# Kernel optimization log

Measured on AMD Instinct MI355X. Metric: run time of the kernel, lower is better.

## Reference

```python
import jax, jax.numpy as jnp
import numpy as np
import math

B, L, D, H, FF = 4, 1024, 1024, 16, 4096
DH = D // H
EPS = 1e-12


def layer_norm(x, gamma, beta):
    mean = x.mean(-1, keepdims=True)
    var = ((x - mean) ** 2).mean(-1, keepdims=True)  # biased var, matches unbiased=False
    return gamma * (x - mean) / jnp.sqrt(var + EPS) + beta


def setup_inputs() -> dict:
    key = jax.random.key(0)
    ks = jax.random.split(key, 16)
    s = 0.02
    return {
        "x": jax.random.normal(ks[0], (B, L, D), jnp.float32),
        "attn_bias": jax.random.uniform(ks[1], (B, L, L), jnp.float32),
        "src_mask": jax.random.randint(ks[2], (B, L), 0, 2, jnp.int32),
        "wq": jax.random.normal(ks[3], (D, D), jnp.float32) * s,
        "bq": jnp.zeros((D,), jnp.float32),
        "wk": jax.random.normal(ks[4], (D, D), jnp.float32) * s,
        "bk": jnp.zeros((D,), jnp.float32),
        "wv": jax.random.normal(ks[5], (D, D), jnp.float32) * s,
        "bv": jnp.zeros((D,), jnp.float32),
        "wo": jax.random.normal(ks[6], (D, D), jnp.float32) * s,
        "bo": jnp.zeros((D,), jnp.float32),
        "gamma1": jnp.ones((D,), jnp.float32),
        "beta1": jnp.zeros((D,), jnp.float32),
        "w1": jax.random.normal(ks[7], (D, FF), jnp.float32) * s,
        "b1": jnp.zeros((FF,), jnp.float32),
        "w2": jax.random.normal(ks[8], (FF, D), jnp.float32) * s,
        "b2": jnp.zeros((D,), jnp.float32),
        "gamma2": jnp.ones((D,), jnp.float32),
        "beta2": jnp.zeros((D,), jnp.float32),
    }


def reference(x, attn_bias, src_mask, wq, bq, wk, bk, wv, bv, wo, bo,
              gamma1, beta1, w1, b1, w2, b2, gamma2, beta2):
    # ---- multi-head attention with multiplicative bias + additive mask ----
    def split_heads(t):  # [B,L,D] -> [B,H,L,DH]
        return t.reshape(B, L, H, DH).transpose(0, 2, 1, 3)

    q = split_heads(x @ wq + bq)
    k = split_heads(x @ wk + bk)
    v = split_heads(x @ wv + bv)

    score = jnp.einsum('bhqd,bhkd->bhqk', q, k) / math.sqrt(DH)
    score = score * attn_bias[:, None, :, :]               # multiplicative bias
    score = jnp.where(src_mask[:, None, None, :] == 0, -10000.0, score)
    p = jax.nn.softmax(score, axis=-1)
    ctx = jnp.einsum('bhqk,bhkd->bhqd', p, v)
    ctx = ctx.transpose(0, 2, 1, 3).reshape(B, L, D)
    attn_out = ctx @ wo + bo

    h = layer_norm(x + attn_out, gamma1, beta1)

    # ---- position-wise FFN ----
    ffn = jax.nn.relu(h @ w1 + b1) @ w2 + b2
    out = layer_norm(h + ffn, gamma2, beta2)
    return out
```

## Files before the change

kernel.cpp:

```cpp
#include <hip/hip_runtime.h>
#include <hip/hip_bf16.h>
#include <math.h>

#define BB 4
#define LL 1024
#define DD 1024
#define HH 16
#define DHH 64
#define FFF 4096
#define MM (BB*LL)
#define LDQ 3072

typedef __attribute__((ext_vector_type(8))) short short8;
typedef __attribute__((ext_vector_type(4))) float f32x4;

__device__ __forceinline__ ushort f2bf(float f) {
    __hip_bfloat16 h = __float2bfloat16(f);
    return *(ushort*)&h;
}
__device__ __forceinline__ float bf2f(ushort u) {
    __hip_bfloat16 h = *(__hip_bfloat16*)&u;
    return __bfloat162float(h);
}
__device__ __forceinline__ float fexp2(float x) {
#if __has_builtin(__builtin_amdgcn_exp2f)
    return __builtin_amdgcn_exp2f(x);
#else
    return exp2f(x);
#endif
}

__device__ __forceinline__ float block_reduce_sum(float v, float* red, int tid) {
    red[tid] = v;
    __syncthreads();
    for (int off = 128; off > 0; off >>= 1) {
        if (tid < off) red[tid] += red[tid + off];
        __syncthreads();
    }
    float r = red[0];
    __syncthreads();
    return r;
}

__global__ __launch_bounds__(256)
void cast_bf16(const float* __restrict__ in, ushort* __restrict__ out) {
    const int i = blockIdx.x * 256 + threadIdx.x;
    float4 v = ((const float4*)in)[i];
    ushort4 o;
    o.x = f2bf(v.x); o.y = f2bf(v.y); o.z = f2bf(v.z); o.w = f2bf(v.w);
    ((ushort4*)out)[i] = o;
}

__global__ __launch_bounds__(256)
void swizzle_bias(const float* __restrict__ bias, float* __restrict__ B) {
    __shared__ float rowbuf[1024];
    const int row = blockIdx.x;
    const int t = threadIdx.x;
    *(float4*)&rowbuf[t * 4] = *(const float4*)&bias[(size_t)row * 1024 + t * 4];
    __syncthreads();
    const int kt = t >> 4, c = t & 15;
    const float s = 1.4426950408889634f;
    float4 o;
    o.x = rowbuf[kt * 64 + 0 * 16 + c] * s;
    o.y = rowbuf[kt * 64 + 1 * 16 + c] * s;
    o.z = rowbuf[kt * 64 + 2 * 16 + c] * s;
    o.w = rowbuf[kt * 64 + 3 * 16 + c] * s;
    *(float4*)&B[(size_t)row * 1024 + t * 4] = o;
}

__global__ __launch_bounds__(256)
void transpose_cast(const float* __restrict__ W, ushort* __restrict__ WT,
                    int K, int N) {
    __shared__ float tile[32][33];
    const int n0 = blockIdx.x * 32, k0 = blockIdx.y * 32;
    const int t = threadIdx.x;
    const int r = t >> 3, c4 = (t & 7) * 4;
    float4 v = *(const float4*)&W[(size_t)(k0 + r) * N + n0 + c4];
    tile[r][c4 + 0] = v.x; tile[r][c4 + 1] = v.y;
    tile[r][c4 + 2] = v.z; tile[r][c4 + 3] = v.w;
    __syncthreads();
    ushort4 o;
    o.x = f2bf(tile[c4 + 0][r]);
    o.y = f2bf(tile[c4 + 1][r]);
    o.z = f2bf(tile[c4 + 2][r]);
    o.w = f2bf(tile[c4 + 3][r]);
    *(ushort4*)&WT[(size_t)(n0 + r) * K + k0 + c4] = o;
}

__global__ __launch_bounds__(256)
void concat3(const float* __restrict__ a, const float* __restrict__ b,
             const float* __restrict__ c, float* __restrict__ o) {
    const int i = blockIdx.x * 256 + threadIdx.x;
    o[i] = (i < 1024) ? a[i] : ((i < 2048) ? b[i - 1024] : c[i - 2048]);
}

template<int BN>
__global__ __launch_bounds__(256)
void gemm_bf16(const ushort* __restrict__ A, const ushort* __restrict__ Bt,
               const float* __restrict__ bias, void* __restrict__ C,
               ushort* __restrict__ Vt, int vn0,
               int M, int N, int K, int relu, int obf16, int qlim) {
    constexpr int JF = BN / 32;
    __shared__ ushort Als0[128 * 32];
    __shared__ ushort Als1[128 * 32];
    __shared__ ushort Bls0[BN * 32];
    __shared__ ushort Bls1[BN * 32];

    const int L = blockIdx.x + gridDim.x * blockIdx.y;
    const int xcd = L & 7;
    const int idx = L >> 3;
    const int mpx = gridDim.y >> 3;
    const int bm = (xcd * mpx + (idx % mpx)) * 128;
    const int bn = (idx / mpx) * BN;

    const int t = threadIdx.x;
    const int lane = t & 63;
    const int w = t >> 6;
    const int wm = (w >> 1) * 64;
    const int wn = (w & 1) * (BN / 2);
    const int fm = lane & 15;
    const int kg = lane >> 4;

    f32x4 acc[4][JF] = {};

    for (int k0 = 0; k0 < K; k0 += 64) {
        #pragma unroll
        for (int j = 0; j < 2; ++j) {
            const int chunk = j * 256 + t;
            const int row = chunk >> 2, kc = chunk & 3;
            const ushort* ga0 = A + (size_t)(bm + row) * K + k0 + kc * 8;
            __builtin_amdgcn_global_load_lds(
                (const __attribute__((address_space(1))) void*)ga0,
                (__attribute__((address_space(3))) void*)(Als0 + chunk * 8), 16, 0, 0);
            const ushort* ga1 = ga0 + 32;
            __builtin_amdgcn_global_load_lds(
                (const __attribute__((address_space(1))) void*)ga1,
                (__attribute__((address_space(3))) void*)(Als1 + chunk * 8), 16, 0, 0);
        }
        #pragma unroll
        for (int j = 0; j < BN / 64; ++j) {
            const int chunk = j * 256 + t;
            const int row = chunk >> 2, kc = chunk & 3;
            const ushort* gb0 = Bt + (size_t)(bn + row) * K + k0 + kc * 8;
            __builtin_amdgcn_global_load_lds(
                (const __attribute__((address_space(1))) void*)gb0,
                (__attribute__((address_space(3))) void*)(Bls0 + chunk * 8), 16, 0, 0);
            const ushort* gb1 = gb0 + 32;
            __builtin_amdgcn_global_load_lds(
                (const __attribute__((address_space(1))) void*)gb1,
                (__attribute__((address_space(3))) void*)(Bls1 + chunk * 8), 16, 0, 0);
        }
        __syncthreads();

        short8 af[4][2], bfr[JF][2];
        #pragma unroll
        for (int i = 0; i < 4; ++i) {
            af[i][0] = *(const short8*)&Als0[(wm + i * 16 + fm) * 32 + kg * 8];
            af[i][1] = *(const short8*)&Als1[(wm + i * 16 + fm) * 32 + kg * 8];
        }
        #pragma unroll
        for (int j = 0; j < JF; ++j) {
            bfr[j][0] = *(const short8*)&Bls0[(wn + j * 16 + fm) * 32 + kg * 8];
            bfr[j][1] = *(const short8*)&Bls1[(wn + j * 16 + fm) * 32 + kg * 8];
        }
        #pragma unroll
        for (int i = 0; i < 4; ++i)
            #pragma unroll
            for (int j = 0; j < JF; ++j) {
                acc[i][j] = __builtin_amdgcn_mfma_f32_16x16x32_bf16(
                    af[i][0], bfr[j][0], acc[i][j], 0, 0, 0);
                acc[i][j] = __builtin_amdgcn_mfma_f32_16x16x32_bf16(
                    af[i][1], bfr[j][1], acc[i][j], 0, 0, 0);
            }
        __syncthreads();
    }

    const int orow0 = (lane >> 4) * 4;
    const int ocol = lane & 15;
    #pragma unroll
    for (int j = 0; j < JF; ++j) {
        const int n = bn + wn + j * 16 + ocol;
        const float bv = bias[n];
        const bool isV = (bn + wn + j * 16) >= vn0;
        #pragma unroll
        for (int i = 0; i < 4; ++i) {
            const int m0 = bm + wm + i * 16 + orow0;
            if (isV) {
                ushort4 o;
                float v0 = acc[i][j][0] + bv, v1 = acc[i][j][1] + bv;
                float v2 = acc[i][j][2] + bv, v3 = acc[i][j][3] + bv;
                o.x = f2bf(v0); o.y = f2bf(v1); o.z = f2bf(v2); o.w = f2bf(v3);
                *(ushort4*)&Vt[((size_t)((m0 >> 10) << 10) + (n - vn0)) * 1024 + (m0 & 1023)] = o;
            } else {
                #pragma unroll
                for (int r = 0; r < 4; ++r) {
                    const int m = m0 + r;
                    float v = acc[i][j][r] + bv;
                    if (relu) v = fmaxf(v, 0.0f);
                    if (n < qlim) v *= 0.125f;
                    if (obf16)
                        ((ushort*)C)[(size_t)m * N + n] = f2bf(v);
                    else
                        ((float*)C)[(size_t)m * N + n] = v;
                }
            }
        }
    }
}

template<int BN>
__global__ __launch_bounds__(256)
void gemm_bf16_sk(const ushort* __restrict__ A, const ushort* __restrict__ Bt,
                  float* __restrict__ P, int M, int N, int K) {
    constexpr int JF = BN / 32;
    __shared__ ushort Als0[128 * 32];
    __shared__ ushort Als1[128 * 32];
    __shared__ ushort Bls0[BN * 32];
    __shared__ ushort Bls1[BN * 32];

    const int L = blockIdx.x + gridDim.x * blockIdx.y;
    const int xcd = L & 7;
    const int idx = L >> 3;
    const int mpx = gridDim.y >> 3;
    const int bm = (xcd * mpx + (idx % mpx)) * 128;
    const int bn = (idx / mpx) * BN;
    const int kbeg = blockIdx.z * (K >> 1);
    const int kend = kbeg + (K >> 1);

    const int t = threadIdx.x;
    const int lane = t & 63;
    const int w = t >> 6;
    const int wm = (w >> 1) * 64;
    const int wn = (w & 1) * (BN / 2);
    const int fm = lane & 15;
    const int kg = lane >> 4;

    f32x4 acc[4][JF] = {};

    for (int k0 = kbeg; k0 < kend; k0 += 64) {
        #pragma unroll
        for (int j = 0; j < 2; ++j) {
            const int chunk = j * 256 + t;
            const int row = chunk >> 2, kc = chunk & 3;
            const ushort* ga0 = A + (size_t)(bm + row) * K + k0 + kc * 8;
            __builtin_amdgcn_global_load_lds(
                (const __attribute__((address_space(1))) void*)ga0,
                (__attribute__((address_space(3))) void*)(Als0 + chunk * 8), 16, 0, 0);
            const ushort* ga1 = ga0 + 32;
            __builtin_amdgcn_global_load_lds(
                (const __attribute__((address_space(1))) void*)ga1,
                (__attribute__((address_space(3))) void*)(Als1 + chunk * 8), 16, 0, 0);
        }
        #pragma unroll
        for (int j = 0; j < BN / 64; ++j) {
            const int chunk = j * 256 + t;
            const int row = chunk >> 2, kc = chunk & 3;
            const ushort* gb0 = Bt + (size_t)(bn + row) * K + k0 + kc * 8;
            __builtin_amdgcn_global_load_lds(
                (const __attribute__((address_space(1))) void*)gb0,
                (__attribute__((address_space(3))) void*)(Bls0 + chunk * 8), 16, 0, 0);
            const ushort* gb1 = gb0 + 32;
            __builtin_amdgcn_global_load_lds(
                (const __attribute__((address_space(1))) void*)gb1,
                (__attribute__((address_space(3))) void*)(Bls1 + chunk * 8), 16, 0, 0);
        }
        __syncthreads();

        short8 af[4][2], bfr[JF][2];
        #pragma unroll
        for (int i = 0; i < 4; ++i) {
            af[i][0] = *(const short8*)&Als0[(wm + i * 16 + fm) * 32 + kg * 8];
            af[i][1] = *(const short8*)&Als1[(wm + i * 16 + fm) * 32 + kg * 8];
        }
        #pragma unroll
        for (int j = 0; j < JF; ++j) {
            bfr[j][0] = *(const short8*)&Bls0[(wn + j * 16 + fm) * 32 + kg * 8];
            bfr[j][1] = *(const short8*)&Bls1[(wn + j * 16 + fm) * 32 + kg * 8];
        }
        #pragma unroll
        for (int i = 0; i < 4; ++i)
            #pragma unroll
            for (int j = 0; j < JF; ++j) {
                acc[i][j] = __builtin_amdgcn_mfma_f32_16x16x32_bf16(
                    af[i][0], bfr[j][0], acc[i][j], 0, 0, 0);
                acc[i][j] = __builtin_amdgcn_mfma_f32_16x16x32_bf16(
                    af[i][1], bfr[j][1], acc[i][j], 0, 0, 0);
            }
        __syncthreads();
    }

    float* Pz = P + (size_t)blockIdx.z * M * N;
    const int orow0 = (lane >> 4) * 4;
    const int ocol = lane & 15;
    #pragma unroll
    for (int j = 0; j < JF; ++j) {
        const int n = bn + wn + j * 16 + ocol;
        #pragma unroll
        for (int i = 0; i < 4; ++i) {
            const int m0 = bm + wm + i * 16 + orow0;
            #pragma unroll
            for (int r = 0; r < 4; ++r)
                Pz[(size_t)(m0 + r) * N + n] = acc[i][j][r];
        }
    }
}

__global__ __launch_bounds__(256, 4)
void attn_mfma(const ushort* __restrict__ QKVb, const ushort* __restrict__ Vt,
               const float* __restrict__ biasw, const int* __restrict__ mask,
               ushort* __restrict__ ctx) {
    const int q0 = blockIdx.x * 64;
    const int h = blockIdx.y;
    const int b = blockIdx.z;
    const int t = threadIdx.x;
    const int lane = t & 63;
    const int w = t >> 6;
    const int g = lane >> 4;
    const int c = lane & 15;

    __shared__ ushort QP[64 * 72];
    __shared__ ushort Ks[64 * 72];
    __shared__ ushort Vs[64 * 72];
    __shared__ float maskS[LL];

    #pragma unroll
    for (int i = 0; i < 2; ++i) {
        const int chunk = i * 256 + t;
        const int row = chunk >> 3, c8 = (chunk & 7) * 8;
        *(short8*)&QP[row * 72 + c8] =
            *(const short8*)(QKVb + ((size_t)(b * LL + q0 + row)) * LDQ + h * DHH + c8);
    }
    {
        int4 mi = ((const int4*)(mask + b * LL))[t];
        float4 mf;
        mf.x = mi.x ? 0.0f : -49152.0f;
        mf.y = mi.y ? 0.0f : -49152.0f;
        mf.z = mi.z ? 0.0f : -49152.0f;
        mf.w = mi.w ? 0.0f : -49152.0f;
        ((float4*)maskS)[t] = mf;
    }

    short8 pk[2], pv[2];
    #pragma unroll
    for (int i = 0; i < 2; ++i) {
        const int chunk = i * 256 + t;
        const int row = chunk >> 3, c8 = (chunk & 7) * 8;
        pk[i] = *(const short8*)(QKVb + ((size_t)(b * LL + row)) * LDQ + 1024 + h * DHH + c8);
        pv[i] = *(const short8*)(Vt + ((size_t)((b * HH + h) * DHH + row)) * LL + c8);
    }
    __syncthreads();

    short8 aq0 = *(const short8*)&QP[(w * 16 + c) * 72 + g * 8];
    short8 aq1 = *(const short8*)&QP[(w * 16 + c) * 72 + g * 8 + 32];
    ushort* Pw = QP + w * (16 * 72);

    const float* bp = biasw + (size_t)(b * LL + q0 + w * 16 + 4 * g) * 1024 + c * 4;
    float4 pb[4];
    #pragma unroll
    for (int r = 0; r < 4; ++r)
        pb[r] = *(const float4*)(bp + r * 1024);

    float l_run[4] = {0.f, 0.f, 0.f, 0.f};
    f32x4 acc_o[4] = {};

    for (int kt = 0; kt < 16; ++kt) {
        #pragma unroll
        for (int i = 0; i < 2; ++i) {
            const int chunk = i * 256 + t;
            const int row = chunk >> 3, c8 = (chunk & 7) * 8;
            *(short8*)&Ks[row * 72 + c8] = pk[i];
            *(short8*)&Vs[row * 72 + c8] = pv[i];
        }
        __syncthreads();

        if (kt < 15) {
            const int k0n = (kt + 1) * 64;
            #pragma unroll
            for (int i = 0; i < 2; ++i) {
                const int chunk = i * 256 + t;
                const int row = chunk >> 3, c8 = (chunk & 7) * 8;
                pk[i] = *(const short8*)(QKVb + ((size_t)(b * LL + k0n + row)) * LDQ + 1024 + h * DHH + c8);
                pv[i] = *(const short8*)(Vt + ((size_t)((b * HH + h) * DHH + row)) * LL + k0n + c8);
            }
        }

        float4 pbn[4];
        if (kt < 15) {
            #pragma unroll
            for (int r = 0; r < 4; ++r)
                pbn[r] = *(const float4*)(bp + r * 1024 + (kt + 1) * 64);
        }

        float mk[4];
        #pragma unroll
        for (int j = 0; j < 4; ++j) mk[j] = maskS[kt * 64 + j * 16 + c];

        f32x4 accs[4] = {};
        __builtin_amdgcn_s_setprio(1);
        #pragma unroll
        for (int j = 0; j < 4; ++j) {
            short8 bk0 = *(const short8*)&Ks[(j * 16 + c) * 72 + g * 8];
            short8 bk1 = *(const short8*)&Ks[(j * 16 + c) * 72 + g * 8 + 32];
            accs[j] = __builtin_amdgcn_mfma_f32_16x16x32_bf16(aq0, bk0, accs[j], 0, 0, 0);
            accs[j] = __builtin_amdgcn_mfma_f32_16x16x32_bf16(aq1, bk1, accs[j], 0, 0, 0);
        }
        __builtin_amdgcn_s_setprio(0);

        #pragma unroll
        for (int j = 0; j < 4; ++j)
            #pragma unroll
            for (int r = 0; r < 4; ++r) {
                const float pe = fexp2(fmaf(accs[j][r], ((const float*)&pb[r])[j], mk[j]));
                l_run[r] += pe;
                Pw[(4 * g + r) * 72 + j * 16 + c] = f2bf(pe);
            }

        __builtin_amdgcn_s_setprio(1);
        #pragma unroll
        for (int ks = 0; ks < 2; ++ks) {
            short8 ap = *(const short8*)&Pw[c * 72 + ks * 32 + g * 8];
            #pragma unroll
            for (int j = 0; j < 4; ++j) {
                short8 bv8 = *(const short8*)&Vs[(j * 16 + c) * 72 + ks * 32 + g * 8];
                acc_o[j] = __builtin_amdgcn_mfma_f32_16x16x32_bf16(ap, bv8, acc_o[j], 0, 0, 0);
            }
        }
        __builtin_amdgcn_s_setprio(0);

        if (kt < 15) {
            #pragma unroll
            for (int r = 0; r < 4; ++r) pb[r] = pbn[r];
        }
        __syncthreads();
    }

    #pragma unroll
    for (int r = 0; r < 4; ++r) {
        float l = l_run[r];
        #pragma unroll
        for (int d = 1; d < 16; d <<= 1) l += __shfl_xor(l, d);
        const float inv = 1.0f / l;
        #pragma unroll
        for (int j = 0; j < 4; ++j)
            ctx[((size_t)(b * LL + q0 + w * 16 + 4 * g + r)) * DD + h * DHH + j * 16 + c] =
                f2bf(acc_o[j][r] * inv);
    }
}

__global__ __launch_bounds__(256)
void add_ln_kernel(const float* __restrict__ P0, const float* __restrict__ P1,
                   const float* __restrict__ cb, const float* __restrict__ bres,
                   const float* __restrict__ gamma, const float* __restrict__ beta,
                   float* __restrict__ out, ushort* __restrict__ outb) {
    const int row = blockIdx.x;
    const int tid = threadIdx.x;
    __shared__ float red[256];

    const size_t base = (size_t)row * DD;
    float v[4];
    float sum = 0.0f;
    #pragma unroll
    for (int i = 0; i < 4; ++i) {
        const int col = tid + i * 256;
        v[i] = P0[base + col] + P1[base + col] + cb[col] + bres[base + col];
        sum += v[i];
    }
    const float mean = block_reduce_sum(sum, red, tid) * (1.0f / 1024.0f);
    float vs = 0.0f;
    #pragma unroll
    for (int i = 0; i < 4; ++i) {
        const float dlt = v[i] - mean;
        vs += dlt * dlt;
    }
    const float var = block_reduce_sum(vs, red, tid) * (1.0f / 1024.0f);
    const float rstd = rsqrtf(var + 1e-12f);
    #pragma unroll
    for (int i = 0; i < 4; ++i) {
        const int col = tid + i * 256;
        const float o = gamma[col] * (v[i] - mean) * rstd + beta[col];
        out[base + col] = o;
        if (outb) outb[base + col] = f2bf(o);
    }
}

extern "C" void kernel_launch(void* const* d_in, const int* in_sizes, int n_in,
                              void* d_out, int out_size, void* d_ws, size_t ws_size,
                              hipStream_t stream) {
    const float* x         = (const float*)d_in[0];
    const float* attn_bias = (const float*)d_in[1];
    const int*   src_mask  = (const int*)  d_in[2];
    const float* wq = (const float*)d_in[3];
    const float* bq = (const float*)d_in[4];
    const float* wk = (const float*)d_in[5];
    const float* bk = (const float*)d_in[6];
    const float* wv = (const float*)d_in[7];
    const float* bv = (const float*)d_in[8];
    const float* wo = (const float*)d_in[9];
    const float* bo = (const float*)d_in[10];
    const float* gamma1 = (const float*)d_in[11];
    const float* beta1  = (const float*)d_in[12];
    const float* w1 = (const float*)d_in[13];
    const float* b1 = (const float*)d_in[14];
    const float* w2 = (const float*)d_in[15];
    const float* b2 = (const float*)d_in[16];
    const float* gamma2 = (const float*)d_in[17];
    const float* beta2  = (const float*)d_in[18];
    float* out = (float*)d_out;

    const size_t MB = 1024 * 1024;
    char* W = (char*)d_ws;
    ushort* xb    = (ushort*)(W + 0);
    ushort* ctxb  = (ushort*)(W + 0);
    ushort* W1T   = (ushort*)(W + 0);
    ushort* QKVb  = (ushort*)(W + 8 * MB);
    float*  Hb    = (float*) (W + 8 * MB);
    ushort* Hbb   = (ushort*)(W + 24 * MB);
    ushort* W2T   = (ushort*)(W + 24 * MB);
    ushort* F1b   = (ushort*)(W + 32 * MB);
    ushort* Vt    = (ushort*)(W + 40 * MB);
    ushort* WQKVT = (ushort*)(W + 48 * MB);
    ushort* WOT   = (ushort*)(W + 48 * MB);
    float*  bqkv  = (float*) (W + 62 * MB);
    float*  biasw = (float*) (W + 64 * MB);
    float*  P0    = (float*) (W + 64 * MB);

    dim3 blk(256);

    cast_bf16<<<dim3(4096), blk, 0, stream>>>(x, xb);
    swizzle_bias<<<dim3(4096), blk, 0, stream>>>(attn_bias, biasw);
    transpose_cast<<<dim3(32, 32), blk, 0, stream>>>(wq, WQKVT, DD, DD);
    transpose_cast<<<dim3(32, 32), blk, 0, stream>>>(wk, WQKVT + 1024 * 1024, DD, DD);
    transpose_cast<<<dim3(32, 32), blk, 0, stream>>>(wv, WQKVT + 2048 * 1024, DD, DD);
    concat3<<<dim3(12), blk, 0, stream>>>(bq, bk, bv, bqkv);
    gemm_bf16<128><<<dim3(24, 32), blk, 0, stream>>>(xb, WQKVT, bqkv, QKVb,
                                                     Vt, 2048, MM, LDQ, DD, 0, 1, 1024);
    attn_mfma<<<dim3(16, HH, BB), blk, 0, stream>>>(QKVb, Vt, biasw, src_mask, ctxb);
    transpose_cast<<<dim3(32, 32), blk, 0, stream>>>(wo, WOT, DD, DD);
    gemm_bf16_sk<64><<<dim3(16, 32, 2), blk, 0, stream>>>(ctxb, WOT, P0, MM, DD, DD);
    transpose_cast<<<dim3(128, 32), blk, 0, stream>>>(w1, W1T, DD, FFF);
    add_ln_kernel<<<dim3(MM), blk, 0, stream>>>(P0, P0 + (size_t)MM * DD, bo, x,
                                                gamma1, beta1, Hb, Hbb);
    gemm_bf16<128><<<dim3(32, 32), blk, 0, stream>>>(Hbb, W1T, b1, F1b,
                                                     Vt, 1 << 30, MM, FFF, DD, 1, 1, 0);
    transpose_cast<<<dim3(32, 128), blk, 0, stream>>>(w2, W2T, FFF, DD);
    gemm_bf16_sk<64><<<dim3(16, 32, 2), blk, 0, stream>>>(F1b, W2T, P0, MM, DD, FFF);
    add_ln_kernel<<<dim3(MM), blk, 0, stream>>>(P0, P0 + (size_t)MM * DD, b2, Hb,
                                                gamma2, beta2, out, nullptr);
}
```

Before: 381.2 us.

## Add 256x256-tile pipelined MFMA GEMM with direct-to-LDS loads for FFN1

Replaces the 128-tile GEMM for the first FFN projection with a new 512-thread kernel using 256x256 output tiles, double-buffered LDS filled via global_load_lds, XOR-swizzled LDS layout, and interleaved half-tile staging with fine-grained barriers and setprio around MFMA clusters. It also remaps block IDs for L2 locality. The aim is higher data reuse per loaded tile and overlap of global loads with MFMA work. The cost is 128KB of LDS per block, which limits occupancy, plus many barriers that could stall.

Result: no change. 374.6 us (-1.7%).

```diff
diff --git a/kernel.cpp b/kernel.cpp
--- a/kernel.cpp
+++ b/kernel.cpp
@@ -303,6 +303,161 @@
                 Pz[(size_t)(m0 + r) * N + n] = acc[i][j][r];
         }
     }
+}
+
+
+#define BARM() asm volatile("s_barrier" ::: "memory")
+#define VMC4() asm volatile("s_waitcnt vmcnt(4)" ::: "memory")
+#define LGK0() do { asm volatile("s_waitcnt lgkmcnt(0)" ::: "memory"); \
+                    __builtin_amdgcn_sched_barrier(0); } while (0)
+
+__device__ __forceinline__ short8 fragrd(const ushort* h, int row, int s, int kg) {
+    const int cb = ((s << 6) + (kg << 4)) ^ (((row >> 2) & 1) << 5);
+    return *(const short8*)(h + row * 64 + (cb >> 1));
+}
+
+__device__ __forceinline__ void stage_half(const ushort* __restrict__ src,
+                                           int srcK, ushort* ldsh, int t) {
+    #pragma unroll
+    for (int l = 0; l < 2; ++l) {
+        const int chunk = l * 512 + t;
+        const int r = chunk >> 3;
+        const int cb_log = ((chunk & 7) * 16) ^ (((r >> 2) & 1) << 5);
+        const ushort* g = src + (size_t)r * srcK + (cb_log >> 1);
+        __builtin_amdgcn_global_load_lds(
+            (const __attribute__((address_space(1))) void*)g,
+            (__attribute__((address_space(3))) void*)(ldsh + chunk * 8), 16, 0, 0);
+    }
+}
+
+__global__ __launch_bounds__(512, 2)
+void gemm256(const ushort* __restrict__ A, const ushort* __restrict__ Bt,
+             const float* __restrict__ bias, ushort* __restrict__ C,
+             int M, int N, int K, int relu) {
+    __shared__ ushort lds[65536];
+
+    const int nt = K >> 6;
+    const int t = threadIdx.x;
+    const int lane = t & 63;
+    const int w = t >> 6;
+    const int wr = w >> 2, wc = w & 3;
+    const int fm = lane & 15, kg = lane >> 4;
+
+    const int bid = blockIdx.x;
+    const int wg = (bid & 7) * (gridDim.x >> 3) + (bid >> 3);
+    const int bm = (wg & 15) << 8;
+    const int bn = (wg >> 4) << 8;
+
+    ushort* const A0 = lds;
+    ushort* const B0 = lds + 16384;
+    ushort* const A1 = lds + 32768;
+    ushort* const B1 = lds + 49152;
+
+    const ushort* const Ah0 = A0 + wr * 8192;
+    const ushort* const Ah1 = A1 + wr * 8192;
+    const ushort* const Bh0 = B0 + (wc >> 1) * 8192;
+    const ushort* const Bh1 = B1 + (wc >> 1) * 8192;
+    const int brow = (wc & 1) * 64;
+
+    #define ASRC(tt, h) (A  + (size_t)(bm + (h) * 128) * K + (tt) * 64)
+    #define BSRC(tt, h) (Bt + (size_t)(bn + (h) * 128) * K + (tt) * 64)
+
+    f32x4 acc[8][4] = {};
+    short8 af[4][2];
+    short8 bf2[4][2];
+
+    #define RD_A(HP, MI0) do { \
+        _Pragma("unroll") \
+        for (int i = 0; i < 4; ++i) { \
+            const int row = ((MI0) + i) * 16 + fm; \
+            af[i][0] = fragrd((HP), row, 0, kg); \
+            af[i][1] = fragrd((HP), row, 1, kg); \
+        } } while (0)
+
+    #define RD_B(HP, J0) do { \
+        _Pragma("unroll") \
+        for (int jj = 0; jj < 2; ++jj) { \
+            const int row = brow + ((J0) + jj) * 16 + fm; \
+            bf2[(J0) + jj][0] = fragrd((HP), row, 0, kg); \
+            bf2[(J0) + jj][1] = fragrd((HP), row, 1, kg); \
+        } } while (0)
+
+    #define QMFMA(MI0, J0) do { \
+        __builtin_amdgcn_s_setprio(1); \
+        _Pragma("unroll") \
+        for (int i = 0; i < 4; ++i) { \
+            _Pragma("unroll") \
+            for (int jj = 0; jj < 2; ++jj) { \
+                acc[(MI0)+i][(J0)+jj] = __builtin_amdgcn_mfma_f32_16x16x32_bf16( \
+                    af[i][0], bf2[(J0)+jj][0], acc[(MI0)+i][(J0)+jj], 0, 0, 0); \
+                acc[(MI0)+i][(J0)+jj] = __builtin_amdgcn_mfma_f32_16x16x32_bf16( \
+                    af[i][1], bf2[(J0)+jj][1], acc[(MI0)+i][(J0)+jj], 0, 0, 0); \
+            } } \
+        __builtin_amdgcn_s_setprio(0); \
+    } while (0)
+
+    stage_half(BSRC(0, 0), K, B0, t);
+    stage_half(BSRC(0, 1), K, B0 + 8192, t);
+    stage_half(ASRC(0, 0), K, A0, t);
+    stage_half(ASRC(0, 1), K, A0 + 8192, t);
+    stage_half(BSRC(1, 0), K, B1, t);
+    stage_half(BSRC(1, 1), K, B1 + 8192, t);
+    VMC4();
+    BARM();
+
+    for (int it = 0; it < (nt >> 1); ++it) {
+        const int ta = 2 * it;
+        const int tb = ta + 1;
+        const int t2 = min(ta + 2, nt - 1);
+        const int t3 = min(ta + 3, nt - 1);
+
+        RD_A(Ah0, 0); RD_B(Bh0, 0);
+        stage_half(ASRC(tb, 0), K, A1, t);
+        BARM(); LGK0(); QMFMA(0, 0); BARM();
+        RD_B(Bh0, 2);
+        stage_half(ASRC(tb, 1), K, A1 + 8192, t);
+        BARM(); LGK0(); QMFMA(0, 2); BARM();
+        RD_A(Ah0, 4);
+        stage_half(BSRC(t2, 0), K, B0, t);
+        BARM(); LGK0(); QMFMA(4, 2); BARM();
+        stage_half(BSRC(t2, 1), K, B0 + 8192, t);
+        VMC4();
+        BARM(); LGK0(); QMFMA(4, 0); BARM();
+        RD_A(Ah1, 0); RD_B(Bh1, 0);
+        stage_half(ASRC(t2, 0), K, A0, t);
+        BARM(); LGK0(); QMFMA(0, 0); BARM();
+        RD_B(Bh1, 2);
+        stage_half(ASRC(t2, 1), K, A0 + 8192, t);
+        BARM(); LGK0(); QMFMA(0, 2); BARM();
+        RD_A(Ah1, 4);
+        stage_half(BSRC(t3, 0), K, B1, t);
+        BARM(); LGK0(); QMFMA(4, 2); BARM();
+        stage_half(BSRC(t3, 1), K, B1 + 8192, t);
+        VMC4();
+        BARM(); LGK0(); QMFMA(4, 0); BARM();
+    }
+
+    const int oc = lane & 15, og = lane >> 4;
+    #pragma unroll
+    for (int nj = 0; nj < 4; ++nj) {
+        const int n = bn + wc * 64 + nj * 16 + oc;
+        const float bv = bias[n];
+        #pragma unroll
+        for (int mi = 0; mi < 8; ++mi) {
+            const int m0 = bm + wr * 128 + mi * 16 + og * 4;
+            #pragma unroll
+            for (int r = 0; r < 4; ++r) {
+                float v = acc[mi][nj][r] + bv;
+                if (relu) v = fmaxf(v, 0.0f);
+                C[(size_t)(m0 + r) * N + n] = f2bf(v);
+            }
+        }
+    }
+    #undef ASRC
+    #undef BSRC
+    #undef RD_A
+    #undef RD_B
+    #undef QMFMA
 }
 
 __global__ __launch_bounds__(256, 4)
@@ -540,8 +695,7 @@
     transpose_cast<<<dim3(128, 32), blk, 0, stream>>>(w1, W1T, DD, FFF);
     add_ln_kernel<<<dim3(MM), blk, 0, stream>>>(P0, P0 + (size_t)MM * DD, bo, x,
                                                 gamma1, beta1, Hb, Hbb);
-    gemm_bf16<128><<<dim3(32, 32), blk, 0, stream>>>(Hbb, W1T, b1, F1b,
-                                                     Vt, 1 << 30, MM, FFF, DD, 1, 1, 0);
+    gemm256<<<dim3(256), dim3(512), 0, stream>>>(Hbb, W1T, b1, F1b, MM, FFF, DD, 1);
     transpose_cast<<<dim3(32, 128), blk, 0, stream>>>(w2, W2T, FFF, DD);
     gemm_bf16_sk<64><<<dim3(16, 32, 2), blk, 0, stream>>>(F1b, W2T, P0, MM, DD, FFF);
     add_ln_kernel<<<dim3(MM), blk, 0, stream>>>(P0, P0 + (size_t)MM * DD, b2, Hb,
```
